# Optimization experiments

Measured on AMD Instinct MI355X. Metric: run time of the kernel, lower is better.

Reference implementation:

```python
import jax, jax.numpy as jnp
import numpy as np

B, L, D = 8, 128, 768
H = 300              # lstm hidden per direction
WMAX = 5             # max span window
NZ = int(L * 0.5)    # span_pruned_threshold = 0.5
SPAN_W_DIM, DIST_DIM, FF = 20, 128, 150
TARGET_DIM, REL_DIM = 3, 4
SPAN_DIM = 2 * 2 * H + SPAN_W_DIM           # 1220
PAIR_DIM = 2 * SPAN_DIM + DIST_DIM          # 2568


def _span_indices(length, wmax):
    starts, ends = [], []
    for w in range(1, wmax + 1):
        s = np.arange(0, length - w + 1)
        starts.append(s)
        ends.append(s + w - 1)
    return np.concatenate(starts), np.concatenate(ends)

_STARTS_NP, _ENDS_NP = _span_indices(L, WMAX)   # Ns = 5L - 10 = 630
_STARTS = jnp.asarray(_STARTS_NP, jnp.int32)
_ENDS = jnp.asarray(_ENDS_NP, jnp.int32)
_WIDTHS = _ENDS - _STARTS + 1                   # width embedding index = j - i + 1


def setup_inputs() -> dict:
    key = jax.random.key(0)
    ks = jax.random.split(key, 16)
    g = lambda i, shape, s=0.05: jax.random.normal(ks[i], shape, dtype=jnp.float32) * s
    z = lambda *shape: jnp.zeros(shape, jnp.float32)
    return {
        'x': jax.random.normal(ks[0], (B, L, D), dtype=jnp.float32),
        'Wih_f': g(1, (4 * H, D)), 'Whh_f': g(2, (4 * H, H)), 'bih_f': z(4 * H), 'bhh_f': z(4 * H),
        'Wih_b': g(3, (4 * H, D)), 'Whh_b': g(4, (4 * H, H)), 'bih_b': z(4 * H), 'bhh_b': z(4 * H),
        'width_emb': g(5, (512, SPAN_W_DIM), 1.0),
        'dist_emb': g(6, (512, DIST_DIM), 1.0),
        'sw1': g(7, (FF, SPAN_DIM)), 'sb1': z(FF),
        'sw2': g(8, (FF, FF)), 'sb2': z(FF),
        'sw3': g(9, (TARGET_DIM, FF)), 'sb3': z(TARGET_DIM),
        'pw1': g(10, (FF, PAIR_DIM)), 'pb1': z(FF),
        'pw2': g(11, (FF, FF)), 'pb2': z(FF),
        'pw3': g(12, (REL_DIM, FF)), 'pb3': z(REL_DIM),
    }


def _lstm_dir(x_tbd, Wih, Whh, bih, bhh):
    """x_tbd: [L, B, D] -> hidden states [L, B, H] (PyTorch LSTM gate order i,f,g,o)."""
    nb = x_tbd.shape[1]
    xg = jnp.einsum('lbd,gd->lbg', x_tbd, Wih) + bih + bhh  # precompute input projections

    def step(carry, xt):
        h, c = carry
        gates = xt + h @ Whh.T
        i, f, gg, o = jnp.split(gates, 4, axis=-1)
        c = jax.nn.sigmoid(f) * c + jax.nn.sigmoid(i) * jnp.tanh(gg)
        h = jax.nn.sigmoid(o) * jnp.tanh(c)
        return (h, c), h

    init = (jnp.zeros((nb, H), x_tbd.dtype), jnp.zeros((nb, H), x_tbd.dtype))
    _, hs = jax.lax.scan(step, init, xg)
    return hs


def _ffnn(zz, w1, b1, w2, b2, w3, b3):
    zz = jax.nn.relu(zz @ w1.T + b1)
    zz = jax.nn.relu(zz @ w2.T + b2)
    return jax.nn.softmax(zz @ w3.T + b3, axis=-1)


def _forward(x, Wih_f, Whh_f, bih_f, bhh_f, Wih_b, Whh_b, bih_b, bhh_b,
             width_emb, dist_emb, sw1, sb1, sw2, sb2, sw3, sb3,
             pw1, pb1, pw2, pb2, pw3, pb3):
    nb = x.shape[0]
    xt = jnp.swapaxes(x, 0, 1)                                  # [L, B, D]
    hf = _lstm_dir(xt, Wih_f, Whh_f, bih_f, bhh_f)
    hb = _lstm_dir(xt[::-1], Wih_b, Whh_b, bih_b, bhh_b)[::-1]
    out = jnp.swapaxes(jnp.concatenate([hf, hb], -1), 0, 1)     # [B, L, 600]

    # span representation: [h_i ; h_j ; width_emb(j-i+1)] -> [B, Ns, 1220]
    wfeat = jnp.broadcast_to(width_emb[_WIDTHS][None], (nb, _STARTS.shape[0], SPAN_W_DIM))
    spans = jnp.concatenate([out[:, _STARTS_NP], out[:, _ENDS_NP], wfeat], axis=-1)

    spans_probability = _ffnn(spans, sw1, sb1, sw2, sb2, sw3, sb3)  # [B, Ns, 3]

    # topk pruning: ASPECT=1, OPINION=2
    t_idx = jax.lax.top_k(spans_probability[:, :, 1], NZ)[1]    # [B, NZ]
    o_idx = jax.lax.top_k(spans_probability[:, :, 2], NZ)[1]

    # itertools.product order: target varies slowest
    pair_t = jnp.repeat(t_idx, NZ, axis=1)                       # [B, NZ*NZ]
    pair_o = jnp.tile(o_idx, (1, NZ))

    a, b = _STARTS[pair_t], _ENDS[pair_t]
    c, d = _STARTS[pair_o], _ENDS[pair_o]
    dist = jnp.minimum(jnp.abs(b - c), jnp.abs(a - d))           # min(|b-c|, |a-d|)

    t_span = jnp.take_along_axis(spans, pair_t[:, :, None], axis=1)
    o_span = jnp.take_along_axis(spans, pair_o[:, :, None], axis=1)
    candidates = jnp.concatenate([t_span, o_span, dist_emb[dist]], axis=-1)  # [B, NZ^2, 2568]

    candidate_probability = _ffnn(candidates, pw1, pb1, pw2, pb2, pw3, pb3)  # [B, NZ^2, 4]
    return spans_probability, candidate_probability, t_idx, o_idx


def reference(x, Wih_f, Whh_f, bih_f, bhh_f, Wih_b, Whh_b, bih_b, bhh_b,
              width_emb, dist_emb, sw1, sb1, sw2, sb2, sw3, sb3,
              pw1, pb1, pw2, pb2, pw3, pb3):
    sp, cp, t_idx, o_idx = _forward(x, Wih_f, Whh_f, bih_f, bhh_f, Wih_b, Whh_b, bih_b, bhh_b,
                                    width_emb, dist_emb, sw1, sb1, sw2, sb2, sw3, sb3,
                                    pw1, pb1, pw2, pb2, pw3, pb3)
    return (sp, cp, t_idx, o_idx)
```

## Files before the change

kernel.cpp:

```cpp
#include <hip/hip_runtime.h>
#include <stdint.h>
#include <stddef.h>

#define BB   8
#define LL   128
#define DD   768
#define HH   300
#define G4   1200
#define NSP  630
#define FFD  150
#define NZK  64

#define WPD  60
#define JC   5

__device__ __forceinline__ float sigm(float x){ return 1.0f/(1.0f+expf(-x)); }

__device__ __forceinline__ void span_decode(int s, int& w, int& i){
  if      (s < 128){ w=1; i=s; }
  else if (s < 255){ w=2; i=s-128; }
  else if (s < 381){ w=3; i=s-255; }
  else if (s < 506){ w=4; i=s-381; }
  else             { w=5; i=s-506; }
}

__device__ __forceinline__ uint64_t shfl_xor_u64(uint64_t v, int m){
  uint32_t lo = (uint32_t)v, hi = (uint32_t)(v >> 32);
  lo = (uint32_t)__shfl_xor((int)lo, m, 64);
  hi = (uint32_t)__shfl_xor((int)hi, m, 64);
  return ((uint64_t)hi << 32) | lo;
}

__global__ __launch_bounds__(256) void k_xg(
    const float* __restrict__ x,
    const float* __restrict__ WihF, const float* __restrict__ bihF, const float* __restrict__ bhhF,
    const float* __restrict__ WihB, const float* __restrict__ bihB, const float* __restrict__ bhhB,
    float* __restrict__ xg, int* __restrict__ tags)
{
  if (blockIdx.x==0 && blockIdx.y==0 && blockIdx.z==0) {
    for (int i = threadIdx.x; i < 2*60*32; i += 256)
      __hip_atomic_store(&tags[i], 0, __ATOMIC_RELAXED, __HIP_MEMORY_SCOPE_AGENT);
  }
  const int dir = blockIdx.z;
  const float* Wih = dir ? WihB : WihF;
  const float* bi  = dir ? bihB : bihF;
  const float* bh  = dir ? bhhB : bhhF;
  const int r0 = blockIdx.x * 64;
  const int n0 = blockIdx.y * 64;
  __shared__ __align__(16) float As[16*68];
  __shared__ __align__(16) float Bs[16*68];
  const int tid = threadIdx.x;
  const int rl = tid >> 2, kq = tid & 3;
  const int tx = tid & 15, ty = tid >> 4;
  float acc[4][4] = {};
  for (int k0 = 0; k0 < DD; k0 += 16) {
    float4 a4 = make_float4(0.f,0.f,0.f,0.f);
    int ra = r0 + rl;
    if (ra < G4) a4 = *(const float4*)&Wih[ra*DD + k0 + kq*4];
    As[(kq*4+0)*68 + rl] = a4.x;
    As[(kq*4+1)*68 + rl] = a4.y;
    As[(kq*4+2)*68 + rl] = a4.z;
    As[(kq*4+3)*68 + rl] = a4.w;
    int n = n0 + rl; int tt = n >> 3, bb = n & 7;
    float4 b4 = *(const float4*)&x[(bb*LL + tt)*DD + k0 + kq*4];
    Bs[(kq*4+0)*68 + rl] = b4.x;
    Bs[(kq*4+1)*68 + rl] = b4.y;
    Bs[(kq*4+2)*68 + rl] = b4.z;
    Bs[(kq*4+3)*68 + rl] = b4.w;
    __syncthreads();
    #pragma unroll
    for (int kk = 0; kk < 16; ++kk) {
      float4 av = *(const float4*)&As[kk*68 + tx*4];
      float4 bv = *(const float4*)&Bs[kk*68 + ty*4];
      float a_[4] = {av.x,av.y,av.z,av.w};
      float b_[4] = {bv.x,bv.y,bv.z,bv.w};
      #pragma unroll
      for (int i=0;i<4;i++)
        #pragma unroll
        for (int j=0;j<4;j++)
          acc[i][j] = fmaf(a_[i], b_[j], acc[i][j]);
    }
    __syncthreads();
  }
  #pragma unroll
  for (int i=0;i<4;i++){
    int r = r0 + tx*4 + i;
    if (r >= G4) continue;
    float bias = bi[r] + bh[r];
    #pragma unroll
    for (int j=0;j<4;j++){
      int n = n0 + ty*4 + j; int tt = n>>3, bb = n&7;
      xg[((dir*LL + tt)*G4 + r)*8 + bb] = acc[i][j] + bias;
    }
  }
}

__global__ __launch_bounds__(320) void k_lstm(
    const float* __restrict__ WhhF, const float* __restrict__ WhhB,
    const float* __restrict__ xg,
    float* __restrict__ hexf,
    int* __restrict__ tags,
    float* __restrict__ out)
{
  const int wg  = blockIdx.x;
  const int dir = wg / WPD;
  const int wid = wg - dir*WPD;
  const int j0  = wid * JC;
  const float* Whh = dir ? WhhB : WhhF;
  float* hex0 = hexf + (size_t)dir*2432;
  int* tg = tags + dir*60*32;

  __shared__ __align__(16) float hls[8*304 + 16];
  __shared__ int hready;

  const int tid  = threadIdx.x;
  const int wv   = tid >> 6;
  const int lane = tid & 63;
  const int rl   = lane >> 4;
  const int s    = lane & 15;
  const int Rabs = rl*HH + j0 + wv;
  const int bb   = s & 7;

  float4 w4[5];
  #pragma unroll
  for (int q=0;q<5;q++){
    int k = s*20 + q*4;
    if (k + 3 < HH) w4[q] = *(const float4*)&Whh[(size_t)Rabs*HH + k];
    else            w4[q] = make_float4(0.f,0.f,0.f,0.f);
  }
  float creg = 0.f;
  if (tid == 0) hready = 0;
  {
    float4* h4 = (float4*)hls;
    for (int i = tid; i < 612; i += 320) h4[i] = make_float4(0.f,0.f,0.f,0.f);
  }
  __syncthreads();

  float xg_c = xg[((size_t)(dir*LL + (dir ? LL-1 : 0))*G4 + Rabs)*8 + bb];

  for (int t = 0; t < LL; ++t) {
    const int tOrig = dir ? (LL-1 - t) : t;
    float xg_n = 0.f;
    if (t+1 < LL) {
      int tO2 = dir ? (LL-2 - t) : (t+1);
      xg_n = xg[((size_t)(dir*LL + tO2)*G4 + Rabs)*8 + bb];
    }
    if (t > 0) {
      if (wv == 0) {
        if (lane < 60) {
          while (__hip_atomic_load(&tg[lane*32], __ATOMIC_RELAXED,
                                   __HIP_MEMORY_SCOPE_AGENT) < t)
            __builtin_amdgcn_s_sleep(1);
        }
        if (lane == 0) ((volatile int*)&hready)[0] = t;
      } else {
        while (((volatile int*)&hready)[0] < t) __builtin_amdgcn_s_sleep(1);
      }
      if (tid < 304) {
        const float* p0 = hex0 + (size_t)(t&1)*4864 + tid*8;
        float4 v0, v1;
        asm volatile(
          "global_load_dwordx4 %0, %2, off sc0 sc1\n\t"
          "global_load_dwordx4 %1, %3, off sc0 sc1\n\t"
          "s_waitcnt vmcnt(0)"
          : "=v"(v0), "=v"(v1)
          : "v"(p0), "v"(p0 + 4)
          : "memory");
        float4* d = (float4*)&hls[tid*8];
        d[0] = v0; d[1] = v1;
      }
    }
    __syncthreads();
    float p[8];
    {
      const float4* h4 = (const float4*)hls;
      #pragma unroll
      for (int b=0;b<8;b++){
        const float4* hb = h4 + b*76 + s*5;
        float ax=0.f, ay=0.f, az=0.f, aw=0.f;
        #pragma unroll
        for (int q=0;q<5;q++){
          float4 hv = hb[q];
          ax = fmaf(w4[q].x, hv.x, ax);
          ay = fmaf(w4[q].y, hv.y, ay);
          az = fmaf(w4[q].z, hv.z, az);
          aw = fmaf(w4[q].w, hv.w, aw);
        }
        p[b] = (ax+ay)+(az+aw);
      }
    }
    #pragma unroll
    for (int b=0;b<8;b++) p[b] += __shfl_xor(p[b], 8, 64);
    float q4[4];
    #pragma unroll
    for (int b=0;b<4;b++){
      float mine = (s&4) ? p[b+4] : p[b];
      float oth  = (s&4) ? p[b]   : p[b+4];
      q4[b] = mine + __shfl_xor(oth, 4, 64);
    }
    float q2[2];
    #pragma unroll
    for (int b=0;b<2;b++){
      float mine = (s&2) ? q4[b+2] : q4[b];
      float oth  = (s&2) ? q4[b]   : q4[b+2];
      q2[b] = mine + __shfl_xor(oth, 2, 64);
    }
    float gv;
    {
      float mine = (s&1) ? q2[1] : q2[0];
      float oth  = (s&1) ? q2[0] : q2[1];
      gv = mine + __shfl_xor(oth, 1, 64) + xg_c;
    }
    {
      int bsel = lane & 7;
      float g_i = __shfl(gv,      bsel, 64);
      float g_f = __shfl(gv, 16 + bsel, 64);
      float g_g = __shfl(gv, 32 + bsel, 64);
      float g_o = __shfl(gv, 48 + bsel, 64);
      if (lane < 8) {
        int b = lane;
        float ig = sigm(g_i), fg = sigm(g_f), gg = tanhf(g_g), og = sigm(g_o);
        creg = fg * creg + ig * gg;
        float h = og * tanhf(creg);
        out[((size_t)(b*LL + tOrig))*600 + dir*HH + j0 + wv] = h;
        if (t+1 < LL)
          __hip_atomic_store(&hex0[(size_t)((t+1)&1)*4864 + b*304 + j0 + wv], h,
                             __ATOMIC_RELAXED, __HIP_MEMORY_SCOPE_AGENT);
      }
    }
    __syncthreads();
    if (t+1 < LL && tid == 0)
      __hip_atomic_store(&tg[wid*32], t+1,
                         __ATOMIC_RELAXED, __HIP_MEMORY_SCOPE_AGENT);
    xg_c = xg_n;
  }
}

__global__ __launch_bounds__(320) void k_uv(
    const float* __restrict__ out, const float* __restrict__ sw1, float* __restrict__ UV)
{
  const int half = blockIdx.z;
  const int row0 = blockIdx.x * 32;
  __shared__ float As[16*36];
  __shared__ __align__(16) float Wt[16*172];
  const int tid = threadIdx.x;
  const int pg = tid / 20, ng = tid - (tid/20)*20;
  float acc[2][8] = {};
  for (int k0 = 0; k0 < 600; k0 += 16) {
    for (int idx = tid; idx < 512; idx += 320) {
      int p = idx >> 4, kk = idx & 15;
      int k = k0 + kk;
      As[kk*36 + p] = (k < 600) ? out[(row0 + p)*600 + k] : 0.f;
    }
    for (int idx = tid; idx < 16*160; idx += 320) {
      int n = idx >> 4, kk = idx & 15;
      int k = k0 + kk;
      Wt[kk*172 + n] = (n < FFD && k < 600) ? sw1[n*1220 + half*600 + k] : 0.f;
    }
    __syncthreads();
    #pragma unroll
    for (int kk=0;kk<16;kk++){
      float2 a2 = *(const float2*)&As[kk*36 + pg*2];
      float4 w0 = *(const float4*)&Wt[kk*172 + ng*8];
      float4 w1 = *(const float4*)&Wt[kk*172 + ng*8 + 4];
      float a_[2] = {a2.x, a2.y};
      float w_[8] = {w0.x,w0.y,w0.z,w0.w,w1.x,w1.y,w1.z,w1.w};
      #pragma unroll
      for (int i=0;i<2;i++)
        #pragma unroll
        for (int j=0;j<8;j++)
          acc[i][j] = fmaf(a_[i], w_[j], acc[i][j]);
    }
    __syncthreads();
  }
  #pragma unroll
  for (int i=0;i<2;i++){
    int row = row0 + pg*2 + i;
    #pragma unroll
    for (int j=0;j<8;j++){
      int n = ng*8 + j;
      if (n < FFD) UV[row*300 + half*FFD + n] = acc[i][j];
    }
  }
}

__global__ __launch_bounds__(160) void k_const(
    const float* __restrict__ sw1, const float* __restrict__ wemb, float* __restrict__ wcst,
    const float* __restrict__ pw1, const float* __restrict__ demb, float* __restrict__ Zd)
{
  int n = threadIdx.x;
  if (n >= FFD) return;
  if (blockIdx.x < 6) {
    int w = blockIdx.x;
    float a = 0.f;
    for (int k=0;k<20;k++) a = fmaf(sw1[n*1220 + 1200 + k], wemb[w*20 + k], a);
    wcst[w*FFD + n] = a;
  } else {
    int d = blockIdx.x - 6;
    float a = 0.f;
    for (int k=0;k<128;k++) a = fmaf(pw1[n*2568 + 2440 + k], demb[d*128 + k], a);
    Zd[d*FFD + n] = a;
  }
}

__global__ __launch_bounds__(320) void k_spanhead(
    const float* __restrict__ UV, const float* __restrict__ wcst,
    const float* __restrict__ sb1,
    const float* __restrict__ sw2, const float* __restrict__ sb2,
    const float* __restrict__ sw3, const float* __restrict__ sb3,
    float* __restrict__ sp)
{
  const int b  = blockIdx.y;
  const int s0 = blockIdx.x * 64;
  __shared__ __align__(16) float z1T[160*68];
  __shared__ __align__(16) float z2T[160*68];
  __shared__ __align__(16) float Wt[16*172];
  __shared__ float zf[256];
  __shared__ int sI[64], sJ[64], sW[64];
  const int tid = threadIdx.x;
  if (tid < 64) {
    int s = s0 + tid; int w = 1, i0 = 0;
    if (s < NSP) span_decode(s, w, i0);
    sI[tid] = i0; sJ[tid] = i0 + w - 1; sW[tid] = w;
  }
  __syncthreads();
  for (int idx = tid; idx < 64*160; idx += 320) {
    int p = idx / 160, k = idx - p*160;
    float v = 0.f;
    if (k < FFD && (s0 + p) < NSP) {
      v = UV[(b*LL + sI[p])*300 + k] + UV[(b*LL + sJ[p])*300 + FFD + k]
        + wcst[sW[p]*FFD + k] + sb1[k];
      v = fmaxf(v, 0.f);
    }
    z1T[k*68 + p] = v;
  }
  const int pg = tid / 20, ng = tid - (tid/20)*20;
  float acc[4][8] = {};
  for (int kt = 0; kt < 10; ++kt) {
    __syncthreads();
    for (int idx = tid; idx < 16*160; idx += 320) {
      int n = idx >> 4, kk = idx & 15;
      int k = kt*16 + kk;
      Wt[kk*172 + n] = (n < FFD && k < FFD) ? sw2[n*FFD + k] : 0.f;
    }
    __syncthreads();
    #pragma unroll
    for (int kk = 0; kk < 16; ++kk) {
      float4 a4 = *(const float4*)&z1T[(kt*16+kk)*68 + pg*4];
      float4 w0 = *(const float4*)&Wt[kk*172 + ng*8];
      float4 w1 = *(const float4*)&Wt[kk*172 + ng*8 + 4];
      float a_[4] = {a4.x,a4.y,a4.z,a4.w};
      float w_[8] = {w0.x,w0.y,w0.z,w0.w,w1.x,w1.y,w1.z,w1.w};
      #pragma unroll
      for (int i=0;i<4;i++)
        #pragma unroll
        for (int j=0;j<8;j++)
          acc[i][j] = fmaf(a_[i], w_[j], acc[i][j]);
    }
  }
  __syncthreads();
  #pragma unroll
  for (int j=0;j<8;j++){
    int n = ng*8 + j;
    float bn = (n < FFD) ? sb2[n] : 0.f;
    #pragma unroll
    for (int i=0;i<4;i++){
      float v = (n < FFD) ? fmaxf(acc[i][j] + bn, 0.f) : 0.f;
      z2T[n*68 + pg*4 + i] = v;
    }
  }
  __syncthreads();
  if (tid < 256) {
    int p = tid >> 2, c = tid & 3;
    if (c < 3 && (s0 + p) < NSP) {
      float a = sb3[c];
      for (int k=0;k<FFD;k++) a = fmaf(z2T[k*68 + p], sw3[c*FFD + k], a);
      zf[p*4 + c] = a;
    }
  }
  __syncthreads();
  if (tid < 64 && (s0 + tid) < NSP) {
    float z0 = zf[tid*4], z1 = zf[tid*4+1], z2 = zf[tid*4+2];
    float m = fmaxf(z0, fmaxf(z1, z2));
    float e0 = expf(z0-m), e1 = expf(z1-m), e2 = expf(z2-m);
    float inv = 1.f/(e0+e1+e2);
    int s = s0 + tid;
    sp[(b*NSP + s)*3 + 0] = e0*inv;
    sp[(b*NSP + s)*3 + 1] = e1*inv;
    sp[(b*NSP + s)*3 + 2] = e2*inv;
  }
}

__global__ __launch_bounds__(64) void k_topk(
    const float* __restrict__ sp, float* __restrict__ outT, float* __restrict__ outO,
    int* __restrict__ idxw)
{
  const int cls = blockIdx.x >> 3;
  const int b   = blockIdx.x & 7;
  const int lane = threadIdx.x;
  uint64_t key[10];
  #pragma unroll
  for (int q=0;q<10;q++){
    int s = lane + q*64;
    uint32_t bits = 0u;
    if (s < NSP) bits = __float_as_uint(sp[(b*NSP + s)*3 + 1 + cls]);
    key[q] = ((uint64_t)bits << 32) | (uint32_t)(1023 - s);
  }
  float* dst = cls ? outO : outT;
  for (int r = 0; r < NZK; ++r) {
    uint64_t best = key[0];
    #pragma unroll
    for (int q=1;q<10;q++) best = key[q] > best ? key[q] : best;
    #pragma unroll
    for (int off = 32; off > 0; off >>= 1) {
      uint64_t o = shfl_xor_u64(best, off);
      best = o > best ? o : best;
    }
    int sWin = 1023 - (int)(best & 0xFFFFFFFFu);
    if ((sWin & 63) == lane) {
      int qw = sWin >> 6;
      #pragma unroll
      for (int q=0;q<10;q++) if (q == qw) key[q] = 0;
    }
    if (lane == 0) {
      dst[b*NZK + r] = (float)sWin;
      idxw[cls*512 + b*NZK + r] = sWin;
    }
  }
}

__global__ __launch_bounds__(320) void k_zto(
    const float* __restrict__ out, const float* __restrict__ wemb,
    const float* __restrict__ pw1, const int* __restrict__ idxw,
    float* __restrict__ ZTO)
{
  const int wg = blockIdx.x;
  const int cls = wg >> 5;
  const int rem = wg & 31;
  const int b = rem >> 2;
  const int i0 = (rem & 3) * 16;
  __shared__ float As[16*20];
  __shared__ __align__(16) float Wt[16*172];
  __shared__ int sI[16], sJ[16], sW[16];
  const int tid = threadIdx.x;
  if (tid < 16) {
    int S = idxw[cls*512 + b*64 + i0 + tid];
    int w, i_; span_decode(S, w, i_);
    sI[tid] = i_; sJ[tid] = i_ + w - 1; sW[tid] = w;
  }
  const int pg = tid / 20, ng = tid - (tid/20)*20;
  float acc[8] = {};
  __syncthreads();
  for (int k0 = 0; k0 < 1232; k0 += 16) {
    if (tid < 256) {
      int p = tid >> 4, kk = tid & 15;
      int k = k0 + kk;
      float v = 0.f;
      if      (k < 600)  v = out[(b*LL + sI[p])*600 + k];
      else if (k < 1200) v = out[(b*LL + sJ[p])*600 + (k - 600)];
      else if (k < 1220) v = wemb[sW[p]*20 + (k - 1200)];
      As[kk*20 + p] = v;
    }
    for (int idx = tid; idx < 16*160; idx += 320) {
      int n = idx >> 4, kk = idx & 15;
      int k = k0 + kk;
      Wt[kk*172 + n] = (n < FFD && k < 1220) ? pw1[n*2568 + cls*1220 + k] : 0.f;
    }
    __syncthreads();
    #pragma unroll
    for (int kk=0;kk<16;kk++){
      float a = As[kk*20 + pg];
      float4 w0 = *(const float4*)&Wt[kk*172 + ng*8];
      float4 w1 = *(const float4*)&Wt[kk*172 + ng*8 + 4];
      acc[0] = fmaf(a, w0.x, acc[0]);
      acc[1] = fmaf(a, w0.y, acc[1]);
      acc[2] = fmaf(a, w0.z, acc[2]);
      acc[3] = fmaf(a, w0.w, acc[3]);
      acc[4] = fmaf(a, w1.x, acc[4]);
      acc[5] = fmaf(a, w1.y, acc[5]);
      acc[6] = fmaf(a, w1.z, acc[6]);
      acc[7] = fmaf(a, w1.w, acc[7]);
    }
    __syncthreads();
  }
  #pragma unroll
  for (int j=0;j<8;j++){
    int n = ng*8 + j;
    if (n < FFD) ZTO[(cls*512 + b*64 + i0 + pg)*FFD + n] = acc[j];
  }
}

__global__ __launch_bounds__(320) void k_pairhead(
    const float* __restrict__ ZTO, const float* __restrict__ Zd,
    const float* __restrict__ pb1,
    const float* __restrict__ pw2, const float* __restrict__ pb2,
    const float* __restrict__ pw3, const float* __restrict__ pb3,
    const int* __restrict__ idxw,
    float* __restrict__ cp)
{
  const int b  = blockIdx.y;
  const int ti = blockIdx.x;
  __shared__ __align__(16) float z1T[160*68];
  __shared__ __align__(16) float z2T[160*68];
  __shared__ __align__(16) float Wt[16*172];
  __shared__ float zf[256];
  __shared__ int oDist[64];
  const int tid = threadIdx.x;
  const int tS = idxw[b*64 + ti];
  int wT, iT; span_decode(tS, wT, iT);
  const int aT = iT, bT = iT + wT - 1;
  if (tid < 64) {
    int oS = idxw[512 + b*64 + tid];
    int wO, iO; span_decode(oS, wO, iO);
    int d1 = bT - iO;            if (d1 < 0) d1 = -d1;
    int d2 = aT - (iO + wO - 1); if (d2 < 0) d2 = -d2;
    oDist[tid] = d1 < d2 ? d1 : d2;
  }
  __syncthreads();
  const float* ZtRow = ZTO + (b*64 + ti)*FFD;
  for (int idx = tid; idx < 64*160; idx += 320) {
    int p = idx / 160, k = idx - p*160;
    float v = 0.f;
    if (k < FFD) {
      v = ZtRow[k] + ZTO[(512 + b*64 + p)*FFD + k] + Zd[oDist[p]*FFD + k] + pb1[k];
      v = fmaxf(v, 0.f);
    }
    z1T[k*68 + p] = v;
  }
  const int pg = tid / 20, ng = tid - (tid/20)*20;
  float acc[4][8] = {};
  for (int kt = 0; kt < 10; ++kt) {
    __syncthreads();
    for (int idx = tid; idx < 16*160; idx += 320) {
      int n = idx >> 4, kk = idx & 15;
      int k = kt*16 + kk;
      Wt[kk*172 + n] = (n < FFD && k < FFD) ? pw2[n*FFD + k] : 0.f;
    }
    __syncthreads();
    #pragma unroll
    for (int kk = 0; kk < 16; ++kk) {
      float4 a4 = *(const float4*)&z1T[(kt*16+kk)*68 + pg*4];
      float4 w0 = *(const float4*)&Wt[kk*172 + ng*8];
      float4 w1 = *(const float4*)&Wt[kk*172 + ng*8 + 4];
      float a_[4] = {a4.x,a4.y,a4.z,a4.w};
      float w_[8] = {w0.x,w0.y,w0.z,w0.w,w1.x,w1.y,w1.z,w1.w};
      #pragma unroll
      for (int i=0;i<4;i++)
        #pragma unroll
        for (int j=0;j<8;j++)
          acc[i][j] = fmaf(a_[i], w_[j], acc[i][j]);
    }
  }
  __syncthreads();
  #pragma unroll
  for (int j=0;j<8;j++){
    int n = ng*8 + j;
    float bn = (n < FFD) ? pb2[n] : 0.f;
    #pragma unroll
    for (int i=0;i<4;i++){
      float v = (n < FFD) ? fmaxf(acc[i][j] + bn, 0.f) : 0.f;
      z2T[n*68 + pg*4 + i] = v;
    }
  }
  __syncthreads();
  if (tid < 256) {
    int p = tid >> 2, c = tid & 3;
    float a = pb3[c];
    for (int k=0;k<FFD;k++) a = fmaf(z2T[k*68 + p], pw3[c*FFD + k], a);
    zf[tid] = a;
  }
  __syncthreads();
  if (tid < 64) {
    float z0 = zf[tid*4], z1 = zf[tid*4+1], z2 = zf[tid*4+2], z3 = zf[tid*4+3];
    float m = fmaxf(fmaxf(z0,z1), fmaxf(z2,z3));
    float e0 = expf(z0-m), e1 = expf(z1-m), e2 = expf(z2-m), e3 = expf(z3-m);
    float inv = 1.f/(e0+e1+e2+e3);
    float4 o4 = make_float4(e0*inv, e1*inv, e2*inv, e3*inv);
    *(float4*)&cp[(size_t)((b*4096 + ti*64 + tid))*4] = o4;
  }
}

extern "C" void kernel_launch(void* const* d_in, const int* in_sizes, int n_in,
                              void* d_out, int out_size, void* d_ws, size_t ws_size,
                              hipStream_t stream) {
  const float* x    = (const float*)d_in[0];
  const float* WihF = (const float*)d_in[1];
  const float* WhhF = (const float*)d_in[2];
  const float* bihF = (const float*)d_in[3];
  const float* bhhF = (const float*)d_in[4];
  const float* WihB = (const float*)d_in[5];
  const float* WhhB = (const float*)d_in[6];
  const float* bihB = (const float*)d_in[7];
  const float* bhhB = (const float*)d_in[8];
  const float* wemb = (const float*)d_in[9];
  const float* demb = (const float*)d_in[10];
  const float* sw1  = (const float*)d_in[11];
  const float* sb1  = (const float*)d_in[12];
  const float* sw2  = (const float*)d_in[13];
  const float* sb2  = (const float*)d_in[14];
  const float* sw3  = (const float*)d_in[15];
  const float* sb3  = (const float*)d_in[16];
  const float* pw1  = (const float*)d_in[17];
  const float* pb1  = (const float*)d_in[18];
  const float* pw2  = (const float*)d_in[19];
  const float* pb2  = (const float*)d_in[20];
  const float* pw3  = (const float*)d_in[21];
  const float* pb3  = (const float*)d_in[22];

  uint8_t* wsb = (uint8_t*)d_ws;
  int*   tags  = (int*)wsb;
  float* hexf  = (float*)(wsb + 16384);
  float* xg    = (float*)(wsb + 131072);
  float* outh  = xg   + 2457600;
  float* UV    = outh + 614400;
  float* wcst  = UV   + 307200;
  float* Zd    = wcst + 900;
  float* ZTO   = Zd   + 38400;
  int*  idxw   = (int*)(ZTO + 153600);

  float* o   = (float*)d_out;
  float* spO = o;
  float* cpO = o + 15120;
  float* tO  = o + 146192;
  float* oO  = o + 146704;

  k_xg      <<<dim3(19,16,2), 256, 0, stream>>>(x, WihF, bihF, bhhF, WihB, bihB, bhhB, xg, tags);
  k_lstm    <<<dim3(2*WPD), 320, 0, stream>>>(WhhF, WhhB, xg, hexf, tags, outh);
  k_uv      <<<dim3(32,1,2), 320, 0, stream>>>(outh, sw1, UV);
  k_const   <<<dim3(262), 160, 0, stream>>>(sw1, wemb, wcst, pw1, demb, Zd);
  k_spanhead<<<dim3(10,8), 320, 0, stream>>>(UV, wcst, sb1, sw2, sb2, sw3, sb3, spO);
  k_topk    <<<dim3(16),  64, 0, stream>>>(spO, tO, oO, idxw);
  k_zto     <<<dim3(64),  320, 0, stream>>>(outh, wemb, pw1, idxw, ZTO);
  k_pairhead<<<dim3(64,8), 320, 0, stream>>>(ZTO, Zd, pb1, pw2, pb2, pw3, pb3, idxw, cpO);
}
```

Before: 1.210 ms.

## Replace LSTM tag barrier with step-tagged h packets and double-buffered LDS

The persistent LSTM kernel drops its per-workgroup tag counters and single-wave spin barrier. Each hidden value is now published as a 64-bit packet that carries its timestep, and every thread polls its own packets directly. Workgroups double to 640 threads covering 10 hidden units each, with half as many groups, and the LDS h buffer is double-buffered so the trailing __syncthreads goes away. The constant-embedding kernel is folded into an extra z-slice of the xg GEMM launch, saving one launch. The price is twice the polling traffic on 64-bit packets and per-thread spin loops that depend on agent-scope visibility holding.

```diff
diff --git a/kernel.cpp b/kernel.cpp
--- a/kernel.cpp
+++ b/kernel.cpp
@@ -11,8 +11,8 @@
 #define FFD  150
 #define NZK  64
 
-#define WPD  60
-#define JC   5
+#define WPD  30
+#define JC   10
 
 __device__ __forceinline__ float sigm(float x){ return 1.0f/(1.0f+expf(-x)); }
 
@@ -31,15 +31,37 @@
   return ((uint64_t)hi << 32) | lo;
 }
 
+__device__ __forceinline__ float4 cload16(const unsigned long long* p){
+  float4 v;
+  asm volatile("global_load_dwordx4 %0, %1, off sc0 sc1\n\ts_waitcnt vmcnt(0)"
+               : "=v"(v) : "v"(p) : "memory");
+  return v;
+}
+
 __global__ __launch_bounds__(256) void k_xg(
     const float* __restrict__ x,
     const float* __restrict__ WihF, const float* __restrict__ bihF, const float* __restrict__ bhhF,
     const float* __restrict__ WihB, const float* __restrict__ bihB, const float* __restrict__ bhhB,
-    float* __restrict__ xg, int* __restrict__ tags)
+    float* __restrict__ xg,
+    const float* __restrict__ sw1, const float* __restrict__ wemb, float* __restrict__ wcst,
+    const float* __restrict__ pw1, const float* __restrict__ demb, float* __restrict__ Zd)
 {
-  if (blockIdx.x==0 && blockIdx.y==0 && blockIdx.z==0) {
-    for (int i = threadIdx.x; i < 2*60*32; i += 256)
-      __hip_atomic_store(&tags[i], 0, __ATOMIC_RELAXED, __HIP_MEMORY_SCOPE_AGENT);
+  if (blockIdx.z == 2) {
+    int cb = blockIdx.y*19 + blockIdx.x;
+    int n = threadIdx.x;
+    if (n < FFD) {
+      if (cb < 6) {
+        float a = 0.f;
+        for (int k=0;k<20;k++) a = fmaf(sw1[n*1220 + 1200 + k], wemb[cb*20 + k], a);
+        wcst[cb*FFD + n] = a;
+      } else if (cb < 262) {
+        int d = cb - 6;
+        float a = 0.f;
+        for (int k=0;k<128;k++) a = fmaf(pw1[n*2568 + 2440 + k], demb[d*128 + k], a);
+        Zd[d*FFD + n] = a;
+      }
+    }
+    return;
   }
   const int dir = blockIdx.z;
   const float* Wih = dir ? WihB : WihF;
@@ -95,11 +117,10 @@
   }
 }
 
-__global__ __launch_bounds__(320) void k_lstm(
+__global__ __launch_bounds__(640) void k_lstm(
     const float* __restrict__ WhhF, const float* __restrict__ WhhB,
     const float* __restrict__ xg,
-    float* __restrict__ hexf,
-    int* __restrict__ tags,
+    unsigned long long* __restrict__ hpkt,
     float* __restrict__ out)
 {
   const int wg  = blockIdx.x;
@@ -107,18 +128,17 @@
   const int wid = wg - dir*WPD;
   const int j0  = wid * JC;
   const float* Whh = dir ? WhhB : WhhF;
-  float* hex0 = hexf + (size_t)dir*2432;
-  int* tg = tags + dir*60*32;
-
-  __shared__ __align__(16) float hls[8*304 + 16];
-  __shared__ int hready;
+  unsigned long long* hp = hpkt + (size_t)dir*2432;
+
+  __shared__ __align__(16) float hls[2*2448];
 
   const int tid  = threadIdx.x;
   const int wv   = tid >> 6;
   const int lane = tid & 63;
   const int rl   = lane >> 4;
   const int s    = lane & 15;
-  const int Rabs = rl*HH + j0 + wv;
+  const int jj   = j0 + wv;
+  const int Rabs = rl*HH + jj;
   const int bb   = s & 7;
 
   float4 w4[5];
@@ -129,10 +149,9 @@
     else            w4[q] = make_float4(0.f,0.f,0.f,0.f);
   }
   float creg = 0.f;
-  if (tid == 0) hready = 0;
   {
     float4* h4 = (float4*)hls;
-    for (int i = tid; i < 612; i += 320) h4[i] = make_float4(0.f,0.f,0.f,0.f);
+    for (int i = tid; i < 1224; i += 640) h4[i] = make_float4(0.f,0.f,0.f,0.f);
   }
   __syncthreads();
 
@@ -146,48 +165,43 @@
       xg_n = xg[((size_t)(dir*LL + tO2)*G4 + Rabs)*8 + bb];
     }
     if (t > 0) {
-      if (wv == 0) {
-        if (lane < 60) {
-          while (__hip_atomic_load(&tg[lane*32], __ATOMIC_RELAXED,
-                                   __HIP_MEMORY_SCOPE_AGENT) < t)
+      const int par = t & 1;
+      if (tid < 608) {
+        const int f0 = 4*tid;
+        float4 a  = make_float4(0.f,0.f,0.f,0.f);
+        float4 b2 = make_float4(0.f,0.f,0.f,0.f);
+        if ((f0 % 304) != 300) {
+          const unsigned long long* p0 = hp + (size_t)par*4864 + f0;
+          const unsigned want = (unsigned)t;
+          a  = cload16(p0);
+          b2 = cload16(p0 + 2);
+          bool ok0 = (__float_as_uint(a.y)==want)  & (__float_as_uint(a.w)==want);
+          bool ok1 = (__float_as_uint(b2.y)==want) & (__float_as_uint(b2.w)==want);
+          while (!(ok0 & ok1)) {
             __builtin_amdgcn_s_sleep(1);
+            if (!ok0) { a  = cload16(p0);     ok0 = (__float_as_uint(a.y)==want)  & (__float_as_uint(a.w)==want); }
+            if (!ok1) { b2 = cload16(p0 + 2); ok1 = (__float_as_uint(b2.y)==want) & (__float_as_uint(b2.w)==want); }
+          }
         }
-        if (lane == 0) ((volatile int*)&hready)[0] = t;
-      } else {
-        while (((volatile int*)&hready)[0] < t) __builtin_amdgcn_s_sleep(1);
+        *(float4*)&hls[par*2448 + f0] = make_float4(a.x, a.z, b2.x, b2.z);
       }
-      if (tid < 304) {
-        const float* p0 = hex0 + (size_t)(t&1)*4864 + tid*8;
-        float4 v0, v1;
-        asm volatile(
-          "global_load_dwordx4 %0, %2, off sc0 sc1\n\t"
-          "global_load_dwordx4 %1, %3, off sc0 sc1\n\t"
-          "s_waitcnt vmcnt(0)"
-          : "=v"(v0), "=v"(v1)
-          : "v"(p0), "v"(p0 + 4)
-          : "memory");
-        float4* d = (float4*)&hls[tid*8];
-        d[0] = v0; d[1] = v1;
+    }
+    __syncthreads();
+    const float4* h4 = (const float4*)&hls[(t&1)*2448];
+    float p[8];
+    #pragma unroll
+    for (int b=0;b<8;b++){
+      const float4* hb = h4 + b*76 + s*5;
+      float ax=0.f, ay=0.f, az=0.f, aw=0.f;
+      #pragma unroll
+      for (int q=0;q<5;q++){
+        float4 hv = hb[q];
+        ax = fmaf(w4[q].x, hv.x, ax);
+        ay = fmaf(w4[q].y, hv.y, ay);
+        az = fmaf(w4[q].z, hv.z, az);
+        aw = fmaf(w4[q].w, hv.w, aw);
       }
-    }
-    __syncthreads();
-    float p[8];
-    {
-      const float4* h4 = (const float4*)hls;
-      #pragma unroll
-      for (int b=0;b<8;b++){
-        const float4* hb = h4 + b*76 + s*5;
-        float ax=0.f, ay=0.f, az=0.f, aw=0.f;
-        #pragma unroll
-        for (int q=0;q<5;q++){
-          float4 hv = hb[q];
-          ax = fmaf(w4[q].x, hv.x, ax);
-          ay = fmaf(w4[q].y, hv.y, ay);
-          az = fmaf(w4[q].z, hv.z, az);
-          aw = fmaf(w4[q].w, hv.w, aw);
-        }
-        p[b] = (ax+ay)+(az+aw);
-      }
+      p[b] = (ax+ay)+(az+aw);
     }
     #pragma unroll
     for (int b=0;b<8;b++) p[b] += __shfl_xor(p[b], 8, 64);
@@ -222,16 +236,16 @@
         float ig = sigm(g_i), fg = sigm(g_f), gg = tanhf(g_g), og = sigm(g_o);
         creg = fg * creg + ig * gg;
         float h = og * tanhf(creg);
-        out[((size_t)(b*LL + tOrig))*600 + dir*HH + j0 + wv] = h;
-        if (t+1 < LL)
-          __hip_atomic_store(&hex0[(size_t)((t+1)&1)*4864 + b*304 + j0 + wv], h,
+        out[((size_t)(b*LL + tOrig))*600 + dir*HH + jj] = h;
+        if (t+1 < LL) {
+          unsigned long long pkt =
+            ((unsigned long long)(unsigned)(t+1) << 32) |
+            (unsigned long long)__float_as_uint(h);
+          __hip_atomic_store(&hp[(size_t)(((t+1)&1))*4864 + b*304 + jj], pkt,
                              __ATOMIC_RELAXED, __HIP_MEMORY_SCOPE_AGENT);
+        }
       }
     }
-    __syncthreads();
-    if (t+1 < LL && tid == 0)
-      __hip_atomic_store(&tg[wid*32], t+1,
-                         __ATOMIC_RELAXED, __HIP_MEMORY_SCOPE_AGENT);
     xg_c = xg_n;
   }
 }
@@ -281,25 +295,6 @@
       int n = ng*8 + j;
       if (n < FFD) UV[row*300 + half*FFD + n] = acc[i][j];
     }
-  }
-}
-
-__global__ __launch_bounds__(160) void k_const(
-    const float* __restrict__ sw1, const float* __restrict__ wemb, float* __restrict__ wcst,
-    const float* __restrict__ pw1, const float* __restrict__ demb, float* __restrict__ Zd)
-{
-  int n = threadIdx.x;
-  if (n >= FFD) return;
-  if (blockIdx.x < 6) {
-    int w = blockIdx.x;
-    float a = 0.f;
-    for (int k=0;k<20;k++) a = fmaf(sw1[n*1220 + 1200 + k], wemb[w*20 + k], a);
-    wcst[w*FFD + n] = a;
-  } else {
-    int d = blockIdx.x - 6;
-    float a = 0.f;
-    for (int k=0;k<128;k++) a = fmaf(pw1[n*2568 + 2440 + k], demb[d*128 + k], a);
-    Zd[d*FFD + n] = a;
   }
 }
 
@@ -608,8 +603,7 @@
   const float* pb3  = (const float*)d_in[22];
 
   uint8_t* wsb = (uint8_t*)d_ws;
-  int*   tags  = (int*)wsb;
-  float* hexf  = (float*)(wsb + 16384);
+  unsigned long long* hpkt = (unsigned long long*)(wsb + 16384);
   float* xg    = (float*)(wsb + 131072);
   float* outh  = xg   + 2457600;
   float* UV    = outh + 614400;
@@ -624,10 +618,10 @@
   float* tO  = o + 146192;
   float* oO  = o + 146704;
 
-  k_xg      <<<dim3(19,16,2), 256, 0, stream>>>(x, WihF, bihF, bhhF, WihB, bihB, bhhB, xg, tags);
-  k_lstm    <<<dim3(2*WPD), 320, 0, stream>>>(WhhF, WhhB, xg, hexf, tags, outh);
+  k_xg      <<<dim3(19,16,3), 256, 0, stream>>>(x, WihF, bihF, bhhF, WihB, bihB, bhhB, xg,
+                                                sw1, wemb, wcst, pw1, demb, Zd);
+  k_lstm    <<<dim3(2*WPD), 640, 0, stream>>>(WhhF, WhhB, xg, hpkt, outh);
   k_uv      <<<dim3(32,1,2), 320, 0, stream>>>(outh, sw1, UV);
-  k_const   <<<dim3(262), 160, 0, stream>>>(sw1, wemb, wcst, pw1, demb, Zd);
   k_spanhead<<<dim3(10,8), 320, 0, stream>>>(UV, wcst, sb1, sw2, sb2, sw3, sb3, spO);
   k_topk    <<<dim3(16),  64, 0, stream>>>(spO, tO, oO, idxw);
   k_zto     <<<dim3(64),  320, 0, stream>>>(outh, wemb, pw1, idxw, ZTO);
```

Result: slower. 1.489 ms (+23.1%).

## Replace per-step block barrier with per-wave arrival counters and double-buffer LSTM hidden state

Applied to the files above, without the earlier changes.

The recurrent LSTM kernel drops the end-of-step __syncthreads. Each wave now drains its stores and atomically increments its block's tag, and consumers wait for a count of 5*t, one arrival per wave. Shared hidden-state storage is double-buffered by step parity so the next step's copy cannot overwrite data still being read. The padded tail load is halved, and the separate constant-embedding kernel is folded into extra blocks of the xg GEMM launch to save a launch. This shortens the serial critical path of the 128-step recurrence, at the cost of more atomics and subtle memory-ordering assumptions.

```diff
diff --git a/kernel.cpp b/kernel.cpp
--- a/kernel.cpp
+++ b/kernel.cpp
@@ -35,11 +35,30 @@
     const float* __restrict__ x,
     const float* __restrict__ WihF, const float* __restrict__ bihF, const float* __restrict__ bhhF,
     const float* __restrict__ WihB, const float* __restrict__ bihB, const float* __restrict__ bhhB,
-    float* __restrict__ xg, int* __restrict__ tags)
+    float* __restrict__ xg, unsigned int* __restrict__ tags,
+    const float* __restrict__ sw1, const float* __restrict__ wemb, float* __restrict__ wcst,
+    const float* __restrict__ pw1, const float* __restrict__ demb, float* __restrict__ Zd)
 {
+  if (blockIdx.z == 2) {
+    int cb = blockIdx.y*19 + blockIdx.x;
+    int n = threadIdx.x;
+    if (n < FFD) {
+      if (cb < 6) {
+        float a = 0.f;
+        for (int k=0;k<20;k++) a = fmaf(sw1[n*1220 + 1200 + k], wemb[cb*20 + k], a);
+        wcst[cb*FFD + n] = a;
+      } else if (cb < 262) {
+        int d = cb - 6;
+        float a = 0.f;
+        for (int k=0;k<128;k++) a = fmaf(pw1[n*2568 + 2440 + k], demb[d*128 + k], a);
+        Zd[d*FFD + n] = a;
+      }
+    }
+    return;
+  }
   if (blockIdx.x==0 && blockIdx.y==0 && blockIdx.z==0) {
     for (int i = threadIdx.x; i < 2*60*32; i += 256)
-      __hip_atomic_store(&tags[i], 0, __ATOMIC_RELAXED, __HIP_MEMORY_SCOPE_AGENT);
+      __hip_atomic_store(&tags[i], 0u, __ATOMIC_RELAXED, __HIP_MEMORY_SCOPE_AGENT);
   }
   const int dir = blockIdx.z;
   const float* Wih = dir ? WihB : WihF;
@@ -99,7 +118,7 @@
     const float* __restrict__ WhhF, const float* __restrict__ WhhB,
     const float* __restrict__ xg,
     float* __restrict__ hexf,
-    int* __restrict__ tags,
+    unsigned int* __restrict__ tags,
     float* __restrict__ out)
 {
   const int wg  = blockIdx.x;
@@ -108,9 +127,9 @@
   const int j0  = wid * JC;
   const float* Whh = dir ? WhhB : WhhF;
   float* hex0 = hexf + (size_t)dir*2432;
-  int* tg = tags + dir*60*32;
-
-  __shared__ __align__(16) float hls[8*304 + 16];
+  unsigned int* tg = tags + dir*60*32;
+
+  __shared__ __align__(16) float hls[2*2448];
   __shared__ int hready;
 
   const int tid  = threadIdx.x;
@@ -118,7 +137,8 @@
   const int lane = tid & 63;
   const int rl   = lane >> 4;
   const int s    = lane & 15;
-  const int Rabs = rl*HH + j0 + wv;
+  const int jj   = j0 + wv;
+  const int Rabs = rl*HH + jj;
   const int bb   = s & 7;
 
   float4 w4[5];
@@ -132,7 +152,7 @@
   if (tid == 0) hready = 0;
   {
     float4* h4 = (float4*)hls;
-    for (int i = tid; i < 612; i += 320) h4[i] = make_float4(0.f,0.f,0.f,0.f);
+    for (int i = tid; i < 1224; i += 320) h4[i] = make_float4(0.f,0.f,0.f,0.f);
   }
   __syncthreads();
 
@@ -146,10 +166,11 @@
       xg_n = xg[((size_t)(dir*LL + tO2)*G4 + Rabs)*8 + bb];
     }
     if (t > 0) {
+      const unsigned want = 5u*(unsigned)t;
       if (wv == 0) {
         if (lane < 60) {
           while (__hip_atomic_load(&tg[lane*32], __ATOMIC_RELAXED,
-                                   __HIP_MEMORY_SCOPE_AGENT) < t)
+                                   __HIP_MEMORY_SCOPE_AGENT) < want)
             __builtin_amdgcn_s_sleep(1);
         }
         if (lane == 0) ((volatile int*)&hready)[0] = t;
@@ -157,37 +178,44 @@
         while (((volatile int*)&hready)[0] < t) __builtin_amdgcn_s_sleep(1);
       }
       if (tid < 304) {
-        const float* p0 = hex0 + (size_t)(t&1)*4864 + tid*8;
+        const int f0 = tid*8;
+        const float* p0 = hex0 + (size_t)(t&1)*4864 + f0;
         float4 v0, v1;
-        asm volatile(
-          "global_load_dwordx4 %0, %2, off sc0 sc1\n\t"
-          "global_load_dwordx4 %1, %3, off sc0 sc1\n\t"
-          "s_waitcnt vmcnt(0)"
-          : "=v"(v0), "=v"(v1)
-          : "v"(p0), "v"(p0 + 4)
-          : "memory");
-        float4* d = (float4*)&hls[tid*8];
+        if ((f0 % 304) == 296) {
+          asm volatile(
+            "global_load_dwordx4 %0, %1, off sc0 sc1\n\t"
+            "s_waitcnt vmcnt(0)"
+            : "=v"(v0) : "v"(p0) : "memory");
+          v1 = make_float4(0.f,0.f,0.f,0.f);
+        } else {
+          asm volatile(
+            "global_load_dwordx4 %0, %2, off sc0 sc1\n\t"
+            "global_load_dwordx4 %1, %3, off sc0 sc1\n\t"
+            "s_waitcnt vmcnt(0)"
+            : "=v"(v0), "=v"(v1)
+            : "v"(p0), "v"(p0 + 4)
+            : "memory");
+        }
+        float4* d = (float4*)&hls[(t&1)*2448 + f0];
         d[0] = v0; d[1] = v1;
       }
     }
     __syncthreads();
+    const float4* h4 = (const float4*)&hls[(t&1)*2448];
     float p[8];
-    {
-      const float4* h4 = (const float4*)hls;
+    #pragma unroll
+    for (int b=0;b<8;b++){
+      const float4* hb = h4 + b*76 + s*5;
+      float ax=0.f, ay=0.f, az=0.f, aw=0.f;
       #pragma unroll
-      for (int b=0;b<8;b++){
-        const float4* hb = h4 + b*76 + s*5;
-        float ax=0.f, ay=0.f, az=0.f, aw=0.f;
-        #pragma unroll
-        for (int q=0;q<5;q++){
-          float4 hv = hb[q];
-          ax = fmaf(w4[q].x, hv.x, ax);
-          ay = fmaf(w4[q].y, hv.y, ay);
-          az = fmaf(w4[q].z, hv.z, az);
-          aw = fmaf(w4[q].w, hv.w, aw);
-        }
-        p[b] = (ax+ay)+(az+aw);
+      for (int q=0;q<5;q++){
+        float4 hv = hb[q];
+        ax = fmaf(w4[q].x, hv.x, ax);
+        ay = fmaf(w4[q].y, hv.y, ay);
+        az = fmaf(w4[q].z, hv.z, az);
+        aw = fmaf(w4[q].w, hv.w, aw);
       }
+      p[b] = (ax+ay)+(az+aw);
     }
     #pragma unroll
     for (int b=0;b<8;b++) p[b] += __shfl_xor(p[b], 8, 64);
@@ -211,6 +239,7 @@
       float oth  = (s&1) ? q2[0] : q2[1];
       gv = mine + __shfl_xor(oth, 1, 64) + xg_c;
     }
+    float hval = 0.f;
     {
       int bsel = lane & 7;
       float g_i = __shfl(gv,      bsel, 64);
@@ -218,20 +247,20 @@
       float g_g = __shfl(gv, 32 + bsel, 64);
       float g_o = __shfl(gv, 48 + bsel, 64);
       if (lane < 8) {
-        int b = lane;
         float ig = sigm(g_i), fg = sigm(g_f), gg = tanhf(g_g), og = sigm(g_o);
         creg = fg * creg + ig * gg;
-        float h = og * tanhf(creg);
-        out[((size_t)(b*LL + tOrig))*600 + dir*HH + j0 + wv] = h;
+        hval = og * tanhf(creg);
         if (t+1 < LL)
-          __hip_atomic_store(&hex0[(size_t)((t+1)&1)*4864 + b*304 + j0 + wv], h,
+          __hip_atomic_store(&hex0[(size_t)(((t+1)&1))*4864 + lane*304 + jj], hval,
                              __ATOMIC_RELAXED, __HIP_MEMORY_SCOPE_AGENT);
       }
     }
-    __syncthreads();
-    if (t+1 < LL && tid == 0)
-      __hip_atomic_store(&tg[wid*32], t+1,
-                         __ATOMIC_RELAXED, __HIP_MEMORY_SCOPE_AGENT);
+    asm volatile("s_waitcnt vmcnt(0)" ::: "memory");
+    if (t+1 < LL && lane == 0)
+      __hip_atomic_fetch_add(&tg[wid*32], 1u,
+                             __ATOMIC_RELAXED, __HIP_MEMORY_SCOPE_AGENT);
+    if (lane < 8)
+      out[((size_t)(lane*LL + tOrig))*600 + dir*HH + jj] = hval;
     xg_c = xg_n;
   }
 }
@@ -281,25 +310,6 @@
       int n = ng*8 + j;
       if (n < FFD) UV[row*300 + half*FFD + n] = acc[i][j];
     }
-  }
-}
-
-__global__ __launch_bounds__(160) void k_const(
-    const float* __restrict__ sw1, const float* __restrict__ wemb, float* __restrict__ wcst,
-    const float* __restrict__ pw1, const float* __restrict__ demb, float* __restrict__ Zd)
-{
-  int n = threadIdx.x;
-  if (n >= FFD) return;
-  if (blockIdx.x < 6) {
-    int w = blockIdx.x;
-    float a = 0.f;
-    for (int k=0;k<20;k++) a = fmaf(sw1[n*1220 + 1200 + k], wemb[w*20 + k], a);
-    wcst[w*FFD + n] = a;
-  } else {
-    int d = blockIdx.x - 6;
-    float a = 0.f;
-    for (int k=0;k<128;k++) a = fmaf(pw1[n*2568 + 2440 + k], demb[d*128 + k], a);
-    Zd[d*FFD + n] = a;
   }
 }
 
@@ -608,7 +618,7 @@
   const float* pb3  = (const float*)d_in[22];
 
   uint8_t* wsb = (uint8_t*)d_ws;
-  int*   tags  = (int*)wsb;
+  unsigned int* tags = (unsigned int*)wsb;
   float* hexf  = (float*)(wsb + 16384);
   float* xg    = (float*)(wsb + 131072);
   float* outh  = xg   + 2457600;
@@ -624,10 +634,10 @@
   float* tO  = o + 146192;
   float* oO  = o + 146704;
 
-  k_xg      <<<dim3(19,16,2), 256, 0, stream>>>(x, WihF, bihF, bhhF, WihB, bihB, bhhB, xg, tags);
+  k_xg      <<<dim3(19,16,3), 256, 0, stream>>>(x, WihF, bihF, bhhF, WihB, bihB, bhhB, xg, tags,
+                                                sw1, wemb, wcst, pw1, demb, Zd);
   k_lstm    <<<dim3(2*WPD), 320, 0, stream>>>(WhhF, WhhB, xg, hexf, tags, outh);
   k_uv      <<<dim3(32,1,2), 320, 0, stream>>>(outh, sw1, UV);
-  k_const   <<<dim3(262), 160, 0, stream>>>(sw1, wemb, wcst, pw1, demb, Zd);
   k_spanhead<<<dim3(10,8), 320, 0, stream>>>(UV, wcst, sb1, sw2, sb2, sw3, sb3, spO);
   k_topk    <<<dim3(16),  64, 0, stream>>>(spO, tO, oO, idxw);
   k_zto     <<<dim3(64),  320, 0, stream>>>(outh, wemb, pw1, idxw, ZTO);
```

New measurement: 1.468 ms. 21.3% more time.
